# Kernel optimization log

Hardware: AMD Instinct MI355X
Metric: run time of the kernel (lower is better)

## Reference

```python
import jax, jax.numpy as jnp
import numpy as np

B, N, D, H, CD = 2, 2048, 1024, 16, 3
HD = D // H


def setup_inputs() -> dict:
    key = jax.random.key(0)
    ks = jax.random.split(key, 6)
    x = jax.random.normal(ks[0], (B, N, D), dtype=jnp.float32)
    coords = jax.random.normal(ks[1], (B, N, CD), dtype=jnp.float32)
    attn_bias = jax.random.normal(ks[2], (N, N), dtype=jnp.float32) * 0.1
    Wqkv = jax.random.normal(ks[3], (D, 3 * D), dtype=jnp.float32) * (1.0 / np.sqrt(D))
    bqkv = jnp.zeros((3 * D,), dtype=jnp.float32)
    rel_weight = jax.random.normal(ks[4], (H, CD), dtype=jnp.float32) * 0.02
    return {"x": x, "coords": coords, "attn_bias": attn_bias, "Wqkv": Wqkv,
            "bqkv": bqkv, "rel_weight": rel_weight}


def reference(x, coords, attn_bias, Wqkv, bqkv, rel_weight):
    b, n, d = x.shape
    h, hd = H, HD
    qkv = x @ Wqkv + bqkv                       # (B,N,3D)
    q, k, v = jnp.split(qkv, 3, axis=-1)
    # reshape_for_mha: (B,N,D) -> (B,H,N,hd)
    def heads(t):
        return t.reshape(b, n, h, hd).transpose(0, 2, 1, 3)
    qh, kh, vh = heads(q), heads(k), heads(v)
    # coord_proj[b,h,n] = coords[b,n,:] @ rel_weight[h,:]
    coord_proj = jnp.einsum('bnc,hc->bhn', coords.astype(jnp.float32), rel_weight)
    # flex_attention: scale by 1/sqrt(head_dim) BEFORE score_mod
    scores = jnp.einsum('bhqd,bhkd->bhqk', qh, kh) / np.sqrt(hd)
    scores = scores + coord_proj[:, :, :, None] - coord_proj[:, :, None, :]
    scores = scores + attn_bias[None, None, :, :]   # '2d' additive mask bias
    attn = jax.nn.softmax(scores, axis=-1)
    yh = jnp.einsum('bhqk,bhkd->bhqd', attn, vh)    # (B,H,N,hd)
    return yh.transpose(0, 2, 1, 3).reshape(b, n, d)
```

## Files before the change

kernel.cpp:

```cpp
#include <hip/hip_runtime.h>
#include <hip/hip_bf16.h>
#include <math.h>

typedef __hip_bfloat16 bf16;
typedef __bf16  bf16x8 __attribute__((ext_vector_type(8)));
typedef float   f32x4  __attribute__((ext_vector_type(4)));

#define BB 2
#define NN 2048
#define DD 1024
#define HH 16
#define HD 64
#define LOG2E   1.44269504f
#define SCALE_Q 0.18033688f

__device__ __forceinline__ void glds16(const bf16* g, bf16* l) {
    __builtin_amdgcn_global_load_lds((const __attribute__((address_space(1))) void*)g,
                                     (__attribute__((address_space(3))) void*)l, 16, 0, 0);
}
__device__ __forceinline__ unsigned short bfu(float x) {
    bf16 b = __float2bfloat16(x);
    return __builtin_bit_cast(unsigned short, b);
}
__device__ __forceinline__ float ubf(unsigned short u) {
    unsigned v = (unsigned)u << 16;
    return __builtin_bit_cast(float, v);
}

__global__ __launch_bounds__(256) void cast_bf16(const float* __restrict__ in,
                                                 bf16* __restrict__ out) {
    size_t i = ((size_t)blockIdx.x * 256 + threadIdx.x) * 8;
    float4 a = *(const float4*)(in + i);
    float4 b = *(const float4*)(in + i + 4);
    bf16 t[8];
    t[0] = __float2bfloat16(a.x); t[1] = __float2bfloat16(a.y);
    t[2] = __float2bfloat16(a.z); t[3] = __float2bfloat16(a.w);
    t[4] = __float2bfloat16(b.x); t[5] = __float2bfloat16(b.y);
    t[6] = __float2bfloat16(b.z); t[7] = __float2bfloat16(b.w);
    *(int4*)(out + i) = *(int4*)t;
}

__global__ __launch_bounds__(256) void transpose_w(const float* __restrict__ W,
                                                   bf16* __restrict__ Wt) {
    __shared__ bf16 t[64][65];
    const int n0 = blockIdx.x * 64;
    const int k0 = blockIdx.y * 64;
    const int tx = threadIdx.x & 63;
    const int tg = threadIdx.x >> 6;
#pragma unroll
    for (int i = 0; i < 16; ++i) {
        int r = tg + i * 4;
        t[r][tx] = __float2bfloat16(W[(size_t)(k0 + r) * 3072 + n0 + tx]);
    }
    __syncthreads();
#pragma unroll
    for (int i = 0; i < 16; ++i) {
        int r = tg + i * 4;
        Wt[(size_t)(n0 + r) * 1024 + k0 + tx] = t[tx][r];
    }
}

__global__ __launch_bounds__(256) void coordproj(const float* __restrict__ c32,
                                                 const float* __restrict__ r32,
                                                 bf16* __restrict__ cpn) {
    int idx = blockIdx.x * 256 + threadIdx.x;
    int n  = idx & (NN - 1);
    int bh = idx >> 11;
    int h  = bh & (HH - 1);
    int b  = bh >> 4;
    float acc = 0.f;
#pragma unroll
    for (int c = 0; c < 3; ++c)
        acc += c32[(size_t)(b * NN + n) * 3 + c] * r32[h * 3 + c];
    cpn[idx] = __float2bfloat16(-LOG2E * acc);
}

__global__ __launch_bounds__(256) void bias_perm(const float* __restrict__ bias,
                                                 bf16* __restrict__ pb) {
    int t    = blockIdx.x * 256 + threadIdx.x;
    int lane = t & 63;
    int wave = (t >> 6) & 3;
    int kt   = (t >> 8) & 31;
    int Qb   = t >> 13;
    int quad = lane >> 4, l15 = lane & 15;
    bf16 v[32];
#pragma unroll
    for (int j = 0; j < 32; ++j) {
        int qb = j >> 4, g = (j >> 2) & 3, r = j & 3;
        int q = Qb * 128 + wave * 32 + qb * 16 + quad * 4 + r;
        int k = kt * 64 + g * 16 + l15;
        v[j] = __float2bfloat16(LOG2E * bias[(size_t)q * NN + k]);
    }
    int4* dst = (int4*)(pb + (size_t)t * 32);
#pragma unroll
    for (int i = 0; i < 4; ++i) dst[i] = ((int4*)v)[i];
}

__global__ __launch_bounds__(256) void qkv_gemm(const bf16* __restrict__ X,
                                                const bf16* __restrict__ W,
                                                const float* __restrict__ bq,
                                                bf16* __restrict__ qo,
                                                bf16* __restrict__ ko,
                                                bf16* __restrict__ vt) {
    __shared__ __align__(16) bf16 As[128 * 32];
    __shared__ __align__(16) bf16 Bs[128 * 32];
    const int tid  = threadIdx.x;
    const int n0   = blockIdx.x * 128;
    const int m0   = blockIdx.y * 128;
    const int wave = tid >> 6, lane = tid & 63, l15 = lane & 15, quad = lane >> 4;
    const int wm   = wave >> 1, wn = wave & 1;

    f32x4 acc[4][4];
    const f32x4 z4 = {0.f, 0.f, 0.f, 0.f};
#pragma unroll
    for (int i = 0; i < 4; ++i)
#pragma unroll
        for (int j = 0; j < 4; ++j) acc[i][j] = z4;

    for (int kt = 0; kt < 1024; kt += 32) {
        __syncthreads();
#pragma unroll
        for (int j = 0; j < 2; ++j) {
            int s   = (wave * 2 + j) * 64 + lane;
            int row = s >> 2;
            int c   = (s & 3) ^ ((row >> 1) & 3);
            glds16(X + (size_t)(m0 + row) * 1024 + kt + c * 8, As + (wave * 2 + j) * 512);
            glds16(W + (size_t)(n0 + row) * 1024 + kt + c * 8, Bs + (wave * 2 + j) * 512);
        }
        __syncthreads();

        bf16x8 a[4], b[4];
#pragma unroll
        for (int mt = 0; mt < 4; ++mt) {
            int ra = wm * 64 + mt * 16 + l15;
            a[mt] = *(const bf16x8*)&As[ra * 32 + ((quad ^ ((ra >> 1) & 3)) * 8)];
        }
#pragma unroll
        for (int nt = 0; nt < 4; ++nt) {
            int rb = wn * 64 + nt * 16 + l15;
            b[nt] = *(const bf16x8*)&Bs[rb * 32 + ((quad ^ ((rb >> 1) & 3)) * 8)];
        }
#pragma unroll
        for (int mt = 0; mt < 4; ++mt)
#pragma unroll
            for (int nt = 0; nt < 4; ++nt)
                acc[mt][nt] = __builtin_amdgcn_mfma_f32_16x16x32_bf16(a[mt], b[nt], acc[mt][nt], 0, 0, 0);
    }

#pragma unroll
    for (int nt = 0; nt < 4; ++nt) {
        int c    = n0 + wn * 64 + nt * 16 + l15;
        int tsel = c >> 10;
        int rem  = c & 1023;
        int h    = rem >> 6, d = rem & 63;
        float bias = bq[c];
        float qs   = (tsel == 0) ? SCALE_Q : 1.0f;
#pragma unroll
        for (int mt = 0; mt < 4; ++mt)
#pragma unroll
            for (int r = 0; r < 4; ++r) {
                int m = m0 + wm * 64 + mt * 16 + quad * 4 + r;
                int b = m >> 11, n = m & (NN - 1);
                bf16 val = __float2bfloat16((acc[mt][nt][r] + bias) * qs);
                if (tsel == 2)
                    vt[((size_t)(b * HH + h) * HD + d) * NN + n] = val;
                else
                    ((tsel == 1) ? ko : qo)[((size_t)(b * HH + h) * NN + n) * HD + d] = val;
            }
    }
}

__global__ __launch_bounds__(256) void attn(const bf16* __restrict__ Q,
                                            const bf16* __restrict__ K,
                                            const bf16* __restrict__ Vt_g,
                                            const bf16* __restrict__ cpn_g,
                                            const bf16* __restrict__ pb,
                                            float* __restrict__ out) {
    __shared__ __align__(16) bf16 Ks[2][64 * 64];
    __shared__ __align__(16) bf16 Vs[2][64 * 64];
    __shared__ __align__(16) unsigned PsW[4][32 * 36];
    __shared__ __align__(16) bf16 cpl[NN];
    const int tid  = threadIdx.x;
    const int Qb   = blockIdx.x;
    const int bh   = blockIdx.y;
    const int b    = bh >> 4, h = bh & 15;
    const int q0   = Qb * 128;
    const int wave = tid >> 6, lane = tid & 63, l15 = lane & 15, quad = lane >> 4;
    const size_t base = (size_t)bh * NN * HD;

    glds16(cpn_g + bh * NN + (wave * 64 + lane) * 8, cpl + wave * 512);

    bf16x8 qf0[2], qf1[2];
#pragma unroll
    for (int qb = 0; qb < 2; ++qb) {
        int qrow = q0 + wave * 32 + qb * 16 + l15;
        qf0[qb] = *(const bf16x8*)&Q[base + (size_t)qrow * HD + quad * 8];
        qf1[qb] = *(const bf16x8*)&Q[base + (size_t)qrow * HD + 32 + quad * 8];
    }

    {
        int s   = (wave * 2) * 64 + lane;
#pragma unroll
        for (int j = 0; j < 2; ++j) {
            int ss  = s + j * 64;
            int row = ss >> 3;
            int c   = (ss & 7) ^ (row & 7);
            glds16(K    + base + (size_t)row * HD + c * 8,  Ks[0] + (wave * 2 + j) * 512);
            glds16(Vt_g + base + (size_t)row * NN + c * 8,  Vs[0] + (wave * 2 + j) * 512);
        }
    }

    const f32x4 z4 = {0.f, 0.f, 0.f, 0.f};
    float l_loc[2][4];
    f32x4 o[2][4];
#pragma unroll
    for (int qb = 0; qb < 2; ++qb) {
#pragma unroll
        for (int r = 0; r < 4; ++r) l_loc[qb][r] = 0.f;
#pragma unroll
        for (int t = 0; t < 4; ++t) o[qb][t] = z4;
    }

    for (int t = 0; t < 32; ++t) {
        const int cur = t & 1;
        __syncthreads();
        if (t < 31) {
            int kk1 = (t + 1) * 64;
#pragma unroll
            for (int j = 0; j < 2; ++j) {
                int ss  = (wave * 2 + j) * 64 + lane;
                int row = ss >> 3;
                int c   = (ss & 7) ^ (row & 7);
                glds16(K    + base + (size_t)(kk1 + row) * HD + c * 8, Ks[cur ^ 1] + (wave * 2 + j) * 512);
                glds16(Vt_g + base + (size_t)row * NN + kk1 + c * 8,   Vs[cur ^ 1] + (wave * 2 + j) * 512);
            }
        }

        const bf16* bsrc = pb + ((((size_t)Qb * 32 + t) * 4 + wave) * 64 + lane) * 32;
        int4 bi0 = ((const int4*)bsrc)[0];
        int4 bi1 = ((const int4*)bsrc)[1];
        int4 bi2 = ((const int4*)bsrc)[2];
        int4 bi3 = ((const int4*)bsrc)[3];
        int4 biv[4] = {bi0, bi1, bi2, bi3};
        const unsigned short* bv = (const unsigned short*)biv;

        bf16x8 k0[4], k1[4];
#pragma unroll
        for (int g = 0; g < 4; ++g) {
            int krow = g * 16 + l15, sw = krow & 7;
            k0[g] = *(const bf16x8*)&Ks[cur][krow * 64 + ((quad ^ sw) * 8)];
            k1[g] = *(const bf16x8*)&Ks[cur][krow * 64 + (((4 + quad) ^ sw) * 8)];
        }

        f32x4 s[2][4];
#pragma unroll
        for (int qb = 0; qb < 2; ++qb)
#pragma unroll
            for (int g = 0; g < 4; ++g) {
                s[qb][g] = __builtin_amdgcn_mfma_f32_16x16x32_bf16(qf0[qb], k0[g], z4, 0, 0, 0);
                s[qb][g] = __builtin_amdgcn_mfma_f32_16x16x32_bf16(qf1[qb], k1[g], s[qb][g], 0, 0, 0);
            }

        float mg[4];
#pragma unroll
        for (int g = 0; g < 4; ++g)
            mg[g] = __bfloat162float(cpl[t * 64 + g * 16 + l15]);

#pragma unroll
        for (int qb = 0; qb < 2; ++qb) {
            float p[4][4];
#pragma unroll
            for (int g = 0; g < 4; ++g)
#pragma unroll
                for (int r = 0; r < 4; ++r) {
                    float e = __builtin_amdgcn_exp2f(s[qb][g][r] + ubf(bv[qb * 16 + g * 4 + r]) + mg[g]);
                    p[g][r] = e;
                    l_loc[qb][r] += e;
                }
#pragma unroll
            for (int g2 = 0; g2 < 2; ++g2)
#pragma unroll
                for (int r = 0; r < 4; ++r) {
                    unsigned pk = (unsigned)bfu(p[g2][r]) | ((unsigned)bfu(p[g2 + 2][r]) << 16);
                    PsW[wave][(qb * 16 + quad * 4 + r) * 36 + g2 * 16 + l15] = pk;
                }
        }
        asm volatile("s_waitcnt lgkmcnt(0)" ::: "memory");

#pragma unroll
        for (int qb = 0; qb < 2; ++qb) {
            const int4* pr = (const int4*)&PsW[wave][(qb * 16 + l15) * 36 + quad * 8];
            int4 da = pr[0], db = pr[1];
            union { unsigned u[4]; bf16x8 v; } u0, u1;
            u0.u[0] = __builtin_amdgcn_perm(da.y, da.x, 0x05040100u);
            u0.u[1] = __builtin_amdgcn_perm(da.w, da.z, 0x05040100u);
            u0.u[2] = __builtin_amdgcn_perm(db.y, db.x, 0x05040100u);
            u0.u[3] = __builtin_amdgcn_perm(db.w, db.z, 0x05040100u);
            u1.u[0] = __builtin_amdgcn_perm(da.y, da.x, 0x07060302u);
            u1.u[1] = __builtin_amdgcn_perm(da.w, da.z, 0x07060302u);
            u1.u[2] = __builtin_amdgcn_perm(db.y, db.x, 0x07060302u);
            u1.u[3] = __builtin_amdgcn_perm(db.w, db.z, 0x07060302u);
#pragma unroll
            for (int tt = 0; tt < 4; ++tt) {
                int drow = tt * 16 + l15, sw = drow & 7;
                bf16x8 v0 = *(const bf16x8*)&Vs[cur][drow * 64 + ((quad ^ sw) * 8)];
                bf16x8 v1 = *(const bf16x8*)&Vs[cur][drow * 64 + (((4 + quad) ^ sw) * 8)];
                o[qb][tt] = __builtin_amdgcn_mfma_f32_16x16x32_bf16(u0.v, v0, o[qb][tt], 0, 0, 0);
                o[qb][tt] = __builtin_amdgcn_mfma_f32_16x16x32_bf16(u1.v, v1, o[qb][tt], 0, 0, 0);
            }
        }
    }

#pragma unroll
    for (int qb = 0; qb < 2; ++qb)
#pragma unroll
        for (int r = 0; r < 4; ++r) {
#pragma unroll
            for (int d = 1; d < 16; d <<= 1)
                l_loc[qb][r] += __shfl_xor(l_loc[qb][r], d, 64);
            float inv = 1.0f / l_loc[qb][r];
            int qq = q0 + wave * 32 + qb * 16 + quad * 4 + r;
#pragma unroll
            for (int tt = 0; tt < 4; ++tt)
                out[((size_t)(b * NN + qq)) * DD + h * HD + tt * 16 + l15] =
                    o[qb][tt][r] * inv;
        }
}

extern "C" void kernel_launch(void* const* d_in, const int* in_sizes, int n_in,
                              void* d_out, int out_size, void* d_ws, size_t ws_size,
                              hipStream_t stream) {
    const float* x      = (const float*)d_in[0];
    const float* coords = (const float*)d_in[1];
    const float* abias  = (const float*)d_in[2];
    const float* Wqkv   = (const float*)d_in[3];
    const float* bqkv   = (const float*)d_in[4];
    const float* relw   = (const float*)d_in[5];
    float* out = (float*)d_out;

    char* ws = (char*)d_ws;
    bf16* xb  = (bf16*)(ws);
    bf16* qw  = (bf16*)(ws + 8388608);
    bf16* kw  = (bf16*)(ws + 16777216);
    bf16* vt  = (bf16*)(ws + 25165824);
    bf16* Wt  = (bf16*)(ws + 33554432);
    bf16* pb  = (bf16*)(ws + 39845888);
    bf16* cpb = (bf16*)(ws + 48234496);

    cast_bf16  <<<dim3(2048),   256, 0, stream>>>(x, xb);
    transpose_w<<<dim3(48, 16), 256, 0, stream>>>(Wqkv, Wt);
    coordproj  <<<dim3(256),    256, 0, stream>>>(coords, relw, cpb);
    bias_perm  <<<dim3(512),    256, 0, stream>>>(abias, pb);
    qkv_gemm   <<<dim3(24, 32), 256, 0, stream>>>(xb, Wt, bqkv, qw, kw, vt);
    attn       <<<dim3(16, 32), 256, 0, stream>>>(qw, kw, vt, cpb, pb, out);
}
```

Baseline: 218.7 us.

## Fuse prep kernels, transpose V separately, store bias fp32, restructure attn loop

Merges the four preprocessing kernels into one launch, keeps the permuted attention bias in fp32 instead of bf16, and has the QKV GEMM write V row-major followed by a separate tiled transpose kernel. The attention kernel adds a min-blocks-per-SM launch bound, halves the per-wave P scratch by handling one q-block at a time, and hoists the V fragment loads out of the q-block loop. The intent is less launch overhead, coalesced V stores, and a better register/LDS budget for occupancy. In exchange the fp32 bias doubles the bias read traffic and the extra transpose adds a pass over V.

```diff
diff --git a/kernel.cpp b/kernel.cpp
--- a/kernel.cpp
+++ b/kernel.cpp
@@ -22,78 +22,74 @@
     bf16 b = __float2bfloat16(x);
     return __builtin_bit_cast(unsigned short, b);
 }
-__device__ __forceinline__ float ubf(unsigned short u) {
-    unsigned v = (unsigned)u << 16;
-    return __builtin_bit_cast(float, v);
-}
-
-__global__ __launch_bounds__(256) void cast_bf16(const float* __restrict__ in,
-                                                 bf16* __restrict__ out) {
-    size_t i = ((size_t)blockIdx.x * 256 + threadIdx.x) * 8;
-    float4 a = *(const float4*)(in + i);
-    float4 b = *(const float4*)(in + i + 4);
-    bf16 t[8];
-    t[0] = __float2bfloat16(a.x); t[1] = __float2bfloat16(a.y);
-    t[2] = __float2bfloat16(a.z); t[3] = __float2bfloat16(a.w);
-    t[4] = __float2bfloat16(b.x); t[5] = __float2bfloat16(b.y);
-    t[6] = __float2bfloat16(b.z); t[7] = __float2bfloat16(b.w);
-    *(int4*)(out + i) = *(int4*)t;
-}
-
-__global__ __launch_bounds__(256) void transpose_w(const float* __restrict__ W,
-                                                   bf16* __restrict__ Wt) {
-    __shared__ bf16 t[64][65];
-    const int n0 = blockIdx.x * 64;
-    const int k0 = blockIdx.y * 64;
-    const int tx = threadIdx.x & 63;
-    const int tg = threadIdx.x >> 6;
-#pragma unroll
-    for (int i = 0; i < 16; ++i) {
-        int r = tg + i * 4;
-        t[r][tx] = __float2bfloat16(W[(size_t)(k0 + r) * 3072 + n0 + tx]);
-    }
-    __syncthreads();
-#pragma unroll
-    for (int i = 0; i < 16; ++i) {
-        int r = tg + i * 4;
-        Wt[(size_t)(n0 + r) * 1024 + k0 + tx] = t[tx][r];
-    }
-}
-
-__global__ __launch_bounds__(256) void coordproj(const float* __restrict__ c32,
-                                                 const float* __restrict__ r32,
-                                                 bf16* __restrict__ cpn) {
-    int idx = blockIdx.x * 256 + threadIdx.x;
-    int n  = idx & (NN - 1);
-    int bh = idx >> 11;
-    int h  = bh & (HH - 1);
-    int b  = bh >> 4;
-    float acc = 0.f;
-#pragma unroll
-    for (int c = 0; c < 3; ++c)
-        acc += c32[(size_t)(b * NN + n) * 3 + c] * r32[h * 3 + c];
-    cpn[idx] = __float2bfloat16(-LOG2E * acc);
-}
-
-__global__ __launch_bounds__(256) void bias_perm(const float* __restrict__ bias,
-                                                 bf16* __restrict__ pb) {
-    int t    = blockIdx.x * 256 + threadIdx.x;
-    int lane = t & 63;
-    int wave = (t >> 6) & 3;
-    int kt   = (t >> 8) & 31;
-    int Qb   = t >> 13;
-    int quad = lane >> 4, l15 = lane & 15;
-    bf16 v[32];
-#pragma unroll
-    for (int j = 0; j < 32; ++j) {
-        int qb = j >> 4, g = (j >> 2) & 3, r = j & 3;
-        int q = Qb * 128 + wave * 32 + qb * 16 + quad * 4 + r;
-        int k = kt * 64 + g * 16 + l15;
-        v[j] = __float2bfloat16(LOG2E * bias[(size_t)q * NN + k]);
-    }
-    int4* dst = (int4*)(pb + (size_t)t * 32);
-#pragma unroll
-    for (int i = 0; i < 4; ++i) dst[i] = ((int4*)v)[i];
+
+__global__ __launch_bounds__(256) void prep(const float* __restrict__ x,
+                                            const float* __restrict__ bias,
+                                            const float* __restrict__ W,
+                                            const float* __restrict__ coords,
+                                            const float* __restrict__ relw,
+                                            bf16* __restrict__ xb,
+                                            float* __restrict__ pbf,
+                                            bf16* __restrict__ Wt,
+                                            bf16* __restrict__ cpn) {
+    __shared__ bf16 tsm[64][65];
+    const int bid = blockIdx.x, tid = threadIdx.x;
+    if (bid < 2048) {
+        size_t i = ((size_t)bid * 256 + tid) * 8;
+        float4 a = *(const float4*)(x + i);
+        float4 b = *(const float4*)(x + i + 4);
+        bf16 t[8];
+        t[0] = __float2bfloat16(a.x); t[1] = __float2bfloat16(a.y);
+        t[2] = __float2bfloat16(a.z); t[3] = __float2bfloat16(a.w);
+        t[4] = __float2bfloat16(b.x); t[5] = __float2bfloat16(b.y);
+        t[6] = __float2bfloat16(b.z); t[7] = __float2bfloat16(b.w);
+        *(int4*)(xb + i) = *(int4*)t;
+    } else if (bid < 2560) {
+        int t    = (bid - 2048) * 256 + tid;
+        int lane = t & 63;
+        int wave = (t >> 6) & 3;
+        int kt   = (t >> 8) & 31;
+        int Qb   = t >> 13;
+        int quad = lane >> 4, l15 = lane & 15;
+        float v[32];
+#pragma unroll
+        for (int j = 0; j < 32; ++j) {
+            int qb = j >> 4, g = (j >> 2) & 3, r = j & 3;
+            int q = Qb * 128 + wave * 32 + qb * 16 + quad * 4 + r;
+            int k = kt * 64 + g * 16 + l15;
+            v[j] = LOG2E * bias[(size_t)q * NN + k];
+        }
+        int4* dst = (int4*)(pbf + (size_t)t * 32);
+#pragma unroll
+        for (int i = 0; i < 8; ++i) dst[i] = ((int4*)v)[i];
+    } else if (bid < 3328) {
+        int idx = bid - 2560;
+        int n0 = (idx % 48) * 64;
+        int k0 = (idx / 48) * 64;
+        int tx = tid & 63, tg = tid >> 6;
+#pragma unroll
+        for (int i = 0; i < 16; ++i) {
+            int r = tg + i * 4;
+            tsm[r][tx] = __float2bfloat16(W[(size_t)(k0 + r) * 3072 + n0 + tx]);
+        }
+        __syncthreads();
+#pragma unroll
+        for (int i = 0; i < 16; ++i) {
+            int r = tg + i * 4;
+            Wt[(size_t)(n0 + r) * 1024 + k0 + tx] = tsm[tx][r];
+        }
+    } else {
+        int idx = (bid - 3328) * 256 + tid;
+        int n  = idx & (NN - 1);
+        int bh = idx >> 11;
+        int h  = bh & (HH - 1);
+        int b  = bh >> 4;
+        float acc = 0.f;
+#pragma unroll
+        for (int c = 0; c < 3; ++c)
+            acc += coords[(size_t)(b * NN + n) * 3 + c] * relw[h * 3 + c];
+        cpn[idx] = __float2bfloat16(-LOG2E * acc);
+    }
 }
 
 __global__ __launch_bounds__(256) void qkv_gemm(const bf16* __restrict__ X,
@@ -101,7 +97,7 @@
                                                 const float* __restrict__ bq,
                                                 bf16* __restrict__ qo,
                                                 bf16* __restrict__ ko,
-                                                bf16* __restrict__ vt) {
+                                                bf16* __restrict__ vo) {
     __shared__ __align__(16) bf16 As[128 * 32];
     __shared__ __align__(16) bf16 Bs[128 * 32];
     const int tid  = threadIdx.x;
@@ -155,30 +151,48 @@
         int h    = rem >> 6, d = rem & 63;
         float bias = bq[c];
         float qs   = (tsel == 0) ? SCALE_Q : 1.0f;
+        bf16* outp = (tsel == 0) ? qo : ((tsel == 1) ? ko : vo);
 #pragma unroll
         for (int mt = 0; mt < 4; ++mt)
 #pragma unroll
             for (int r = 0; r < 4; ++r) {
                 int m = m0 + wm * 64 + mt * 16 + quad * 4 + r;
                 int b = m >> 11, n = m & (NN - 1);
-                bf16 val = __float2bfloat16((acc[mt][nt][r] + bias) * qs);
-                if (tsel == 2)
-                    vt[((size_t)(b * HH + h) * HD + d) * NN + n] = val;
-                else
-                    ((tsel == 1) ? ko : qo)[((size_t)(b * HH + h) * NN + n) * HD + d] = val;
+                outp[((size_t)(b * HH + h) * NN + n) * HD + d] =
+                    __float2bfloat16((acc[mt][nt][r] + bias) * qs);
             }
     }
 }
 
-__global__ __launch_bounds__(256) void attn(const bf16* __restrict__ Q,
-                                            const bf16* __restrict__ K,
-                                            const bf16* __restrict__ Vt_g,
-                                            const bf16* __restrict__ cpn_g,
-                                            const bf16* __restrict__ pb,
-                                            float* __restrict__ out) {
+__global__ __launch_bounds__(256) void transpose_v(const bf16* __restrict__ vw,
+                                                   bf16* __restrict__ vt) {
+    __shared__ bf16 t[64][65];
+    const int bh = blockIdx.y;
+    const int n0 = blockIdx.x * 64;
+    const size_t base = (size_t)bh * NN * HD;
+    const int tx = threadIdx.x & 63, tg = threadIdx.x >> 6;
+#pragma unroll
+    for (int i = 0; i < 16; ++i) {
+        int r = tg + i * 4;
+        t[r][tx] = vw[base + (size_t)(n0 + r) * HD + tx];
+    }
+    __syncthreads();
+#pragma unroll
+    for (int i = 0; i < 16; ++i) {
+        int d = tg + i * 4;
+        vt[base + (size_t)d * NN + n0 + tx] = t[tx][d];
+    }
+}
+
+__global__ __launch_bounds__(256, 3) void attn(const bf16* __restrict__ Q,
+                                               const bf16* __restrict__ K,
+                                               const bf16* __restrict__ Vt_g,
+                                               const bf16* __restrict__ cpn_g,
+                                               const float* __restrict__ pbf,
+                                               float* __restrict__ out) {
     __shared__ __align__(16) bf16 Ks[2][64 * 64];
     __shared__ __align__(16) bf16 Vs[2][64 * 64];
-    __shared__ __align__(16) unsigned PsW[4][32 * 36];
+    __shared__ __align__(16) unsigned PsW[4][16 * 36];
     __shared__ __align__(16) bf16 cpl[NN];
     const int tid  = threadIdx.x;
     const int Qb   = blockIdx.x;
@@ -198,16 +212,13 @@
         qf1[qb] = *(const bf16x8*)&Q[base + (size_t)qrow * HD + 32 + quad * 8];
     }
 
-    {
-        int s   = (wave * 2) * 64 + lane;
-#pragma unroll
-        for (int j = 0; j < 2; ++j) {
-            int ss  = s + j * 64;
-            int row = ss >> 3;
-            int c   = (ss & 7) ^ (row & 7);
-            glds16(K    + base + (size_t)row * HD + c * 8,  Ks[0] + (wave * 2 + j) * 512);
-            glds16(Vt_g + base + (size_t)row * NN + c * 8,  Vs[0] + (wave * 2 + j) * 512);
-        }
+#pragma unroll
+    for (int j = 0; j < 2; ++j) {
+        int ss  = (wave * 2 + j) * 64 + lane;
+        int row = ss >> 3;
+        int c   = (ss & 7) ^ (row & 7);
+        glds16(K    + base + (size_t)row * HD + c * 8,  Ks[0] + (wave * 2 + j) * 512);
+        glds16(Vt_g + base + (size_t)row * NN + c * 8,  Vs[0] + (wave * 2 + j) * 512);
     }
 
     const f32x4 z4 = {0.f, 0.f, 0.f, 0.f};
@@ -236,14 +247,6 @@
             }
         }
 
-        const bf16* bsrc = pb + ((((size_t)Qb * 32 + t) * 4 + wave) * 64 + lane) * 32;
-        int4 bi0 = ((const int4*)bsrc)[0];
-        int4 bi1 = ((const int4*)bsrc)[1];
-        int4 bi2 = ((const int4*)bsrc)[2];
-        int4 bi3 = ((const int4*)bsrc)[3];
-        int4 biv[4] = {bi0, bi1, bi2, bi3};
-        const unsigned short* bv = (const unsigned short*)biv;
-
         bf16x8 k0[4], k1[4];
 #pragma unroll
         for (int g = 0; g < 4; ++g) {
@@ -266,14 +269,29 @@
         for (int g = 0; g < 4; ++g)
             mg[g] = __bfloat162float(cpl[t * 64 + g * 16 + l15]);
 
+        bf16x8 v0[4], v1[4];
+#pragma unroll
+        for (int tt = 0; tt < 4; ++tt) {
+            int drow = tt * 16 + l15, sw = drow & 7;
+            v0[tt] = *(const bf16x8*)&Vs[cur][drow * 64 + ((quad ^ sw) * 8)];
+            v1[tt] = *(const bf16x8*)&Vs[cur][drow * 64 + (((4 + quad) ^ sw) * 8)];
+        }
+
+        const float* bsrc = pbf + ((((size_t)Qb * 32 + t) * 4 + wave) * 64 + lane) * 32;
+
 #pragma unroll
         for (int qb = 0; qb < 2; ++qb) {
+            float4 bv[4];
+#pragma unroll
+            for (int i = 0; i < 4; ++i) bv[i] = ((const float4*)(bsrc + qb * 16))[i];
+            const float* bf = (const float*)bv;
+
             float p[4][4];
 #pragma unroll
             for (int g = 0; g < 4; ++g)
 #pragma unroll
                 for (int r = 0; r < 4; ++r) {
-                    float e = __builtin_amdgcn_exp2f(s[qb][g][r] + ubf(bv[qb * 16 + g * 4 + r]) + mg[g]);
+                    float e = __builtin_amdgcn_exp2f(s[qb][g][r] + bf[g * 4 + r] + mg[g]);
                     p[g][r] = e;
                     l_loc[qb][r] += e;
                 }
@@ -282,14 +300,10 @@
 #pragma unroll
                 for (int r = 0; r < 4; ++r) {
                     unsigned pk = (unsigned)bfu(p[g2][r]) | ((unsigned)bfu(p[g2 + 2][r]) << 16);
-                    PsW[wave][(qb * 16 + quad * 4 + r) * 36 + g2 * 16 + l15] = pk;
+                    PsW[wave][(quad * 4 + r) * 36 + g2 * 16 + l15] = pk;
                 }
-        }
-        asm volatile("s_waitcnt lgkmcnt(0)" ::: "memory");
-
-#pragma unroll
-        for (int qb = 0; qb < 2; ++qb) {
-            const int4* pr = (const int4*)&PsW[wave][(qb * 16 + l15) * 36 + quad * 8];
+            asm volatile("s_waitcnt lgkmcnt(0)" ::: "memory");
+            const int4* pr = (const int4*)&PsW[wave][l15 * 36 + quad * 8];
             int4 da = pr[0], db = pr[1];
             union { unsigned u[4]; bf16x8 v; } u0, u1;
             u0.u[0] = __builtin_amdgcn_perm(da.y, da.x, 0x05040100u);
@@ -302,11 +316,8 @@
             u1.u[3] = __builtin_amdgcn_perm(db.w, db.z, 0x07060302u);
 #pragma unroll
             for (int tt = 0; tt < 4; ++tt) {
-                int drow = tt * 16 + l15, sw = drow & 7;
-                bf16x8 v0 = *(const bf16x8*)&Vs[cur][drow * 64 + ((quad ^ sw) * 8)];
-                bf16x8 v1 = *(const bf16x8*)&Vs[cur][drow * 64 + (((4 + quad) ^ sw) * 8)];
-                o[qb][tt] = __builtin_amdgcn_mfma_f32_16x16x32_bf16(u0.v, v0, o[qb][tt], 0, 0, 0);
-                o[qb][tt] = __builtin_amdgcn_mfma_f32_16x16x32_bf16(u1.v, v1, o[qb][tt], 0, 0, 0);
+                o[qb][tt] = __builtin_amdgcn_mfma_f32_16x16x32_bf16(u0.v, v0[tt], o[qb][tt], 0, 0, 0);
+                o[qb][tt] = __builtin_amdgcn_mfma_f32_16x16x32_bf16(u1.v, v1[tt], o[qb][tt], 0, 0, 0);
             }
         }
     }
@@ -339,18 +350,18 @@
     float* out = (float*)d_out;
 
     char* ws = (char*)d_ws;
-    bf16* xb  = (bf16*)(ws);
-    bf16* qw  = (bf16*)(ws + 8388608);
-    bf16* kw  = (bf16*)(ws + 16777216);
-    bf16* vt  = (bf16*)(ws + 25165824);
-    bf16* Wt  = (bf16*)(ws + 33554432);
-    bf16* pb  = (bf16*)(ws + 39845888);
-    bf16* cpb = (bf16*)(ws + 48234496);
-
-    cast_bf16  <<<dim3(2048),   256, 0, stream>>>(x, xb);
-    transpose_w<<<dim3(48, 16), 256, 0, stream>>>(Wqkv, Wt);
-    coordproj  <<<dim3(256),    256, 0, stream>>>(coords, relw, cpb);
-    bias_perm  <<<dim3(512),    256, 0, stream>>>(abias, pb);
-    qkv_gemm   <<<dim3(24, 32), 256, 0, stream>>>(xb, Wt, bqkv, qw, kw, vt);
-    attn       <<<dim3(16, 32), 256, 0, stream>>>(qw, kw, vt, cpb, pb, out);
-}
+    bf16*  xb  = (bf16*)(ws);
+    bf16*  vt  = (bf16*)(ws);
+    bf16*  qw  = (bf16*)(ws + 8388608);
+    bf16*  kw  = (bf16*)(ws + 16777216);
+    bf16*  vw  = (bf16*)(ws + 25165824);
+    bf16*  Wt  = (bf16*)(ws + 33554432);
+    float* pbf = (float*)(ws + 39845888);
+    bf16*  cpb = (bf16*)(ws + 56623104);
+
+    prep       <<<dim3(3584),   256, 0, stream>>>(x, abias, Wqkv, coords, relw,
+                                                  xb, pbf, Wt, cpb);
+    qkv_gemm   <<<dim3(24, 32), 256, 0, stream>>>(xb, Wt, bqkv, qw, kw, vw);
+    transpose_v<<<dim3(32, 32), 256, 0, stream>>>(vw, vt);
+    attn       <<<dim3(16, 32), 256, 0, stream>>>(qw, kw, vt, cpb, pbf, out);
+}
```

New measurement: 233.9 us. 6.9% more time.
